# Kernel optimization log

Measured on AMD Instinct MI355X. Metric: run time of the kernel, lower is better.

Reference implementation:

```python
import jax, jax.numpy as jnp
import numpy as np

N, D, S, H, QP, VP = 512, 256, 32, 4, 8, 8
PAIR_C = S + 3 * VP          # 56
P3 = H * QP * 3              # 96
FD = P3 + 16                 # 112 (rel + dist rbf)


def _layer_norm(x, scale, offset, eps=1e-5):
    mu = x.mean(-1, keepdims=True)
    var = ((x - mu) ** 2).mean(-1, keepdims=True)
    return (x - mu) * jax.lax.rsqrt(var + eps) * scale + offset


def _distance_rbf(d, bins=16, min_d=0.0, max_d=22.0):
    # Gaussian RBF featurization of pairwise distances (salad distance_rbf).
    step = (max_d - min_d) / bins
    centers = min_d + step * jnp.arange(bins, dtype=d.dtype) + step / 2
    return jnp.exp(-(((d[..., None] - centers) / step) ** 2))


def setup_inputs() -> dict:
    key = jax.random.key(0)
    ks = jax.random.split(key, 16)
    f32 = jnp.float32
    nrm = lambda k, shape, s=1.0: (s * jax.random.normal(k, shape)).astype(f32)
    HS = H * S
    return {
        "local": nrm(ks[0], (N, D)),
        "pos": nrm(ks[1], (N, 5, 3)),
        "resi": jnp.arange(N, dtype=jnp.int32),
        "chain": jax.random.randint(ks[2], (N,), 0, 2, dtype=jnp.int32),
        "batch": jnp.zeros((N,), dtype=jnp.int32),
        "mask": jnp.ones((N,), dtype=bool),
        "q_ln_scale": jnp.ones((S,), f32),
        "q_ln_offset": jnp.zeros((S,), f32),
        "k_ln_scale": jnp.ones((S,), f32),
        "k_ln_offset": jnp.zeros((S,), f32),
        "w_q": nrm(ks[3], (D, HS), D ** -0.5),
        "b_q": jnp.zeros((HS,), f32),
        "w_k": nrm(ks[4], (D, HS), D ** -0.5),
        "b_k": jnp.zeros((HS,), f32),
        "w_v": nrm(ks[5], (D, HS), D ** -0.5),
        "b_v": jnp.zeros((HS,), f32),
        "w_qp": nrm(ks[6], (D, H * QP * 3), 0.1 * D ** -0.5),
        "b_qp": jnp.zeros((H * QP * 3,), f32),
        "w_kp": nrm(ks[7], (D, H * QP * 3), 0.1 * D ** -0.5),
        "b_kp": jnp.zeros((H * QP * 3,), f32),
        "w_vp": nrm(ks[8], (D, H * VP * 3), 0.1 * D ** -0.5),
        "b_vp": jnp.zeros((H * VP * 3,), f32),
        "resi_embedding": nrm(ks[9], (66, PAIR_C), 66 ** -0.5),
        "w_pair": nrm(ks[10], (FD, PAIR_C), FD ** -0.5),
        "w_bias": nrm(ks[11], (FD, H), FD ** -0.5),
        "b_bias": jnp.zeros((H,), f32),
        "gamma": jnp.full((H,), np.log(np.e - 1.0), f32),
        "w_out": nrm(ks[12], (H * PAIR_C, D), (H * PAIR_C) ** -0.5),
    }


def reference(local, pos, resi, chain, batch, mask,
              q_ln_scale, q_ln_offset, k_ln_scale, k_ln_offset,
              w_q, b_q, w_k, b_k, w_v, b_v,
              w_qp, b_qp, w_kp, b_kp, w_vp, b_vp,
              resi_embedding, w_pair, w_bias, b_bias, gamma, w_out):
    n = local.shape[0]
    ca = pos[:, 1]  # [n,3]

    q = _layer_norm((local @ w_q + b_q).reshape(n, H, S), q_ln_scale, q_ln_offset)
    k = _layer_norm((local @ w_k + b_k).reshape(n, H, S), k_ln_scale, k_ln_offset)
    v = (local @ w_v + b_v).reshape(n, H, S)
    qp = (local @ w_qp + b_qp).reshape(n, H, QP, 3) + ca[:, None, None]
    kp = (local @ w_kp + b_kp).reshape(n, H, QP, 3) + ca[:, None, None]
    vp = (local @ w_vp + b_vp).reshape(n, H, VP, 3) + ca[:, None, None]
    value = jnp.concatenate((v, vp.reshape(n, H, 3 * VP)), axis=-1)  # [n,H,56]

    same_batch = batch[:, None] == batch[None, :]
    pair_mask = (mask[:, None] & mask[None, :]) & same_batch  # [n,n]

    inner = jnp.einsum('ihc,jhc->ijh', q * jnp.sqrt(1.0 / S), k)  # [n,n,H]
    diff = qp[:, None] - kp[None, :]                 # [n,n,H,QP,3]
    point_att = -(diff ** 2).sum(axis=(-1, -2))      # [n,n,H]
    rel = diff.reshape(n, n, P3)                     # [n,n,96]

    dca = 10.0 * ca
    dist = jnp.sqrt(((dca[:, None] - dca[None, :]) ** 2).sum(-1) + 1e-6)
    dist = _distance_rbf(dist)                       # [n,n,16]

    resi_dist = jnp.clip(resi[:, None] - resi[None, :], -32, 32)
    other_chain = chain[:, None] != chain[None, :]
    rdist = jnp.where(other_chain, 65, resi_dist + 32)
    emb = resi_embedding[rdist]                      # [n,n,56]

    feat = jnp.concatenate((rel, dist), axis=-1)     # [n,n,112]
    pair = emb + feat @ w_pair                       # [n,n,56]
    bias = feat @ w_bias + b_bias                    # [n,n,H]
    pair = pair[:, :, None, :] + value[None]         # [n,n,H,56]

    w_C = jnp.sqrt(2.0 / (9 * QP))
    point_scale = jax.nn.softplus(gamma).reshape(1, 1, H) * w_C / 2

    attn = (inner + point_scale * point_att + bias) * jnp.sqrt(1.0 / 3.0)
    attn = jnp.where(pair_mask[..., None], attn, -1e9)
    attn = jax.nn.softmax(attn, axis=1)
    attn = jnp.where(pair_mask[..., None], attn, 0.0)

    result = jnp.einsum('ijh,ijhc->ihc', attn, pair).reshape(n, -1)  # [n,224]
    return result @ w_out                             # [n,D]
```

## Files before the change

### kernel.cpp

```cpp
#include <hip/hip_runtime.h>
#include <hip/hip_bf16.h>
#include <cstddef>

#define N_NODES 512
#define DIM     256
#define H_HEADS 4
#define PAIR_CN 56
#define P3_N    96
#define FD_N    112
#define HPC     224

typedef _Float16 h2v  __attribute__((ext_vector_type(2)));
typedef _Float16 f16x8 __attribute__((ext_vector_type(8)));
typedef float    f32x4 __attribute__((ext_vector_type(4)));

__device__ __forceinline__ bool mask_true(const void* m, int idx) {
    if (((const unsigned char*)m)[idx] != 0) return true;
    return ((const int*)m)[idx] != 0;
}
__device__ __forceinline__ unsigned packh2(float a, float b) {
    _Float16 ha = (_Float16)a, hb = (_Float16)b;
    unsigned short ua, ub;
    __builtin_memcpy(&ua, &ha, 2); __builtin_memcpy(&ub, &hb, 2);
    return (unsigned)ua | ((unsigned)ub << 16);
// ... 115 lines not shown
                const float x6 = xL[r][d0 + 6], x7 = xL[r][d0 + 7];
                acc[r][0] += x0*wv0.x + x1*wv1.x + x2*wv2.x + x3*wv3.x
                           + x4*wv4.x + x5*wv5.x + x6*wv6.x + x7*wv7.x;
                acc[r][1] += x0*wv0.y + x1*wv1.y + x2*wv2.y + x3*wv3.y
                           + x4*wv4.y + x5*wv5.y + x6*wv6.y + x7*wv7.y;
                acc[r][2] += x0*wv0.z + x1*wv1.z + x2*wv2.z + x3*wv3.z
                           + x4*wv4.z + x5*wv5.z + x6*wv6.z + x7*wv7.z;
                acc[r][3] += x0*wv0.w + x1*wv1.w + x2*wv2.w + x3*wv3.w
                           + x4*wv4.w + x5*wv5.w + x6*wv6.w + x7*wv7.w;
            }
        }
#pragma unroll
        for (int r = 0; r < 2; ++r)
#pragma unroll
            for (int e = 0; e < 4; ++e)
                acc[r][e] += __shfl_xor(acc[r][e], 1);

        if (dh == 0) {
            const float cax0 = pos[i0*15+3],     cay0 = pos[i0*15+4],     caz0 = pos[i0*15+5];
            const float cax1 = pos[(i0+1)*15+3], cay1 = pos[(i0+1)*15+4], caz1 = pos[(i0+1)*15+5];
            float fr0[4], fr1[4];
            const bool isKp = (seg == 4), isQp = (seg == 3);
#pragma unroll
            for (int e = 0; e < 4; ++e) {
                const int cc = c + e;
                const float v0 = acc[0][e], v1 = acc[1][e];
                if (seg == 0) {
                    qraw[0][cc] = v0 + b_q[cc];
                    qraw[1][cc] = v1 + b_q[cc];
                } else if (seg == 1) {
                    kraw[0][cc] = v0 + b_k[cc];
                    kraw[1][cc] = v1 + b_k[cc];
                } else if (seg == 2) {
                    const int h = cc >> 5, sc = cc & 31;
                    const int colF = h*PAIR_CN + sc;
                    BF[(colF >> 4)*4096 + (colF & 15)*4 + cstBF] =
                        packh2(v0 + b_v[cc], v1 + b_v[cc]);
                } else if (seg == 3) {
                    const int x = cc % 3;
                    const float cav0 = (x==0)?cax0:((x==1)?cay0:caz0);
                    const float cav1 = (x==0)?cax1:((x==1)?cay1:caz1);
                    const float r0 = v0 + b_qp[cc] + cav0;
                    const float r1 = v1 + b_qp[cc] + cav1;
                    fr0[e] = r0; fr1[e] = r1;
                    qpL[0][cc] = r0; qpL[1][cc] = r1;
                } else if (seg == 4) {
                    const int x = cc % 3;
                    const float cav0 = (x==0)?cax0:((x==1)?cay0:caz0);
                    const float cav1 = (x==0)?cax1:((x==1)?cay1:caz1);
                    const float r0 = v0 + b_kp[cc] + cav0;
                    const float r1 = v1 + b_kp[cc] + cav1;
                    fr0[e] = r0; fr1[e] = r1;
                    const int colF = 224 + cc;
                    BF[(colF >> 4)*4096 + (colF & 15)*4 + cstBF] = packh2(r0, r1);
                    kpbL[0][cc] = (float)(_Float16)r0;
                    kpbL[1][cc] = (float)(_Float16)r1;
                } else {
                    const int h = cc / 24, rr = cc % 24, x = cc % 3;
                    const float cav0 = (x==0)?cax0:((x==1)?cay0:caz0);
                    const float cav1 = (x==0)?cax1:((x==1)?cay1:caz1);
                    const int colF = h*PAIR_CN + 32 + rr;
                    BF[(colF >> 4)*4096 + (colF & 15)*4 + cstBF] =
                        packh2(v0 + b_vp[cc] + cav0, v1 + b_vp[cc] + cav1);
                }
            }
            if (isQp) {
                const int f2 = c >> 1;
                qpP[(size_t)i0*48 + f2]         = packh2(fr0[0], fr0[1]);
                qpP[(size_t)i0*48 + f2 + 1]     = packh2(fr0[2], fr0[3]);
                qpP[(size_t)(i0+1)*48 + f2]     = packh2(fr1[0], fr1[1]);
                qpP[(size_t)(i0+1)*48 + f2 + 1] = packh2(fr1[2], fr1[3]);
            }
            if (isKp) {
                const int f2 = c >> 1;
                const int fq = f2 >> 2;
                kpT4[((size_t)fq*N_NODES + i0    )*4 + (f2 & 3)]       = packh2(fr0[0], fr0[1]);
                kpT4[((size_t)fq*N_NODES + i0    )*4 + ((f2 + 1) & 3)] = packh2(fr0[2], fr0[3]);
                kpT4[((size_t)fq*N_NODES + i0 + 1)*4 + (f2 & 3)]       = packh2(fr1[0], fr1[1]);
                kpT4[((size_t)fq*N_NODES + i0 + 1)*4 + ((f2 + 1) & 3)] = packh2(fr1[2], fr1[3]);
            }
        }
    }
    __syncthreads();

    if (tid < 16) {
        const int r = tid >> 3, t = tid & 7;
        const float* src = (t < 4) ? qraw[r] : kraw[r];
        const int h = t & 3, base = (t < 4) ? 0 : 8;
        float mu = 0.f;
        for (int c = 0; c < 32; ++c) mu += src[h*32 + c];
        mu *= (1.f/32.f);
        float var = 0.f;
        for (int c = 0; c < 32; ++c) { float d = src[h*32 + c] - mu; var += d*d; }
        var *= (1.f/32.f);
        stat[r][base + h*2 + 0] = mu;
        stat[r][base + h*2 + 1] = var;
    }
    __syncthreads();

    {
        const int r = tid >> 8, u = tid & 255;
        const int i = i0 + r;
        if (u < 128) {
            const int h = u >> 5, sidx = u & 31;
            const float mu = stat[r][h*2], var = stat[r][h*2+1];
            float v = (qraw[r][u] - mu) * rsqrtf(var + 1e-5f) * qls[sidx] + qlo[sidx];
            v *= 0.17677669529663687f;
            const float vo = __shfl_xor(v, 1);
            if (!(u & 1)) qnP[(size_t)i*64 + (u >> 1)] = packh2(v, vo);
        } else {
            const int u2 = u - 128, h = u2 >> 5, sidx = u2 & 31;
            const float mu = stat[r][8 + h*2], var = stat[r][9 + h*2];
            float v = (kraw[r][u2] - mu) * rsqrtf(var + 1e-5f) * kls[sidx] + klo[sidx];
            const float vo = __shfl_xor(v, 1);
            if (!(u2 & 1))
                knT4[(((size_t)(u2 >> 3))*N_NODES + i)*4 + ((u2 >> 1) & 3)] = packh2(v, vo);
        }
    }

    if (tid < 64) {
        const int r = tid >> 5, h = (tid >> 3) & 3, ks = tid & 7;
        float uacc = 0.f, tacc = 0.f;
#pragma unroll
        for (int f = ks; f < P3_N; f += 8) {
            float wb = wbS[f*4 + h];
            uacc += qpL[r][f] * wb;
            tacc += kpbL[r][f] * wb;
        }
        float nq = 0.f, nk = 0.f;
#pragma unroll
        for (int f = h*24 + ks*3; f < h*24 + ks*3 + 3; ++f) {
            nq += qpL[r][f]*qpL[r][f];
            nk += kpbL[r][f]*kpbL[r][f];
        }
        uacc += __shfl_xor(uacc,1); uacc += __shfl_xor(uacc,2); uacc += __shfl_xor(uacc,4);
        tacc += __shfl_xor(tacc,1); tacc += __shfl_xor(tacc,2); tacc += __shfl_xor(tacc,4);
        nq   += __shfl_xor(nq,1);   nq   += __shfl_xor(nq,2);   nq   += __shfl_xor(nq,4);
        nk   += __shfl_xor(nk,1);   nk   += __shfl_xor(nk,2);   nk   += __shfl_xor(nk,4);
        if (ks == 0) {
            const int n = i0 + r;
            const float ps = log1pf(expf(gamma[h])) * (1.0f/12.0f);
            iinfo[n*4 + h] = -ps*nq + uacc + b_bias[h];
            jinfo[n*8 + h] = -ps*nk - tacc;
            if (h == 0) {
                jinfo[n*8 + 4] = 10.f * pos[n*15 + 3];
                jinfo[n*8 + 5] = 10.f * pos[n*15 + 4];
                jinfo[n*8 + 6] = 10.f * pos[n*15 + 5];
                jinfo[n*8 + 7] = 0.f;
            }
        }
    }
}

__global__ __launch_bounds__(512, 4) void attn_kernel(
    const unsigned* __restrict__ qnP, const unsigned* __restrict__ knT4,
    const unsigned* __restrict__ qpP, const unsigned* __restrict__ kpT4,
    const unsigned* __restrict__ BF,
    const unsigned* __restrict__ woPk, const unsigned* __restrict__ wp2,
    const unsigned* __restrict__ remb2,
    const float* __restrict__ jinfo, const float* __restrict__ iinfo,
    const int* __restrict__ resi, const int* __restrict__ chain,
    const int* __restrict__ batch, const void* __restrict__ maskp,
    const float* __restrict__ w_bias, const float* __restrict__ gamma,
    float* __restrict__ out)
{
    const int i    = blockIdx.x;
    const int tid  = threadIdx.x;
    const int lane = tid & 63;
    const int wv   = tid >> 6;

    __shared__ unsigned qpkL[64];
    __shared__ unsigned qspkL[48];
    __shared__ unsigned wbPk[H_HEADS][8];
    __shared__ __align__(16) unsigned rbfP[N_NODES][9];
    __shared__ __align__(16) unsigned attnH[H_HEADS][260];
    __shared__ float    mxW[8][H_HEADS], smW[8][H_HEADS];
    __shared__ float    asL[H_HEADS];
    __shared__ float    qpiL[P3_N];
    __shared__ float    GLfF[H_HEADS][P3_N];
    __shared__ float    GLfR[H_HEADS][16];
    __shared__ unsigned GLf2[H_HEADS][56];
    __shared__ unsigned abktP[H_HEADS][33];
    __shared__ float    resL[HPC];
    __shared__ unsigned resH[FD_N];
    __shared__ float    abktW[8][H_HEADS][66];
    __shared__ unsigned char rdL[N_NODES], pmL[N_NODES];

    if (tid < 64) {
        qpkL[tid] = qnP[(size_t)i*64 + tid];
    } else if (tid < 112) {
        const int f2 = tid - 64, h = f2 / 12;
        const float ps2 = 2.f * log1pf(expf(gamma[h])) * (1.0f/12.0f);
        const unsigned u = qpP[(size_t)i*48 + f2];
        qspkL[f2] = packh2(ps2*h2lof(u), ps2*h2hif(u));
    } else if (tid < 160) {
        const int f2 = tid - 112;
        const unsigned u = qpP[(size_t)i*48 + f2];
        qpiL[2*f2]   = h2lof(u);
        qpiL[2*f2+1] = h2hif(u);
    } else if (tid < 192) {
        const int v = tid - 160, h = v >> 3, e = v & 7;
        wbPk[h][e] = packh2(w_bias[(P3_N + 2*e)*H_HEADS + h],
                            w_bias[(P3_N + 2*e + 1)*H_HEADS + h]);
    }
    for (int t = tid; t < 8*H_HEADS*66; t += 512) ((float*)abktW)[t] = 0.f;

    const int  r_i = resi[i], ch_i = chain[i], ba_i = batch[i];
    const bool m_i = mask_true(maskp, i);
    const float dix = jinfo[(size_t)i*8+4], diy = jinfo[(size_t)i*8+5], diz = jinfo[(size_t)i*8+6];

    const float inv3  = 0.57735026918962576f;
    const float rstep = 0.72727272727272727f;

    const int j = tid;
    const float4 vq4 = *(const float4*)(jinfo + (size_t)j*8);
    const float4 dj4 = *(const float4*)(jinfo + (size_t)j*8 + 4);
    const float4 ci4 = *(const float4*)(iinfo + (size_t)i*4);
    const float vqa[4] = {vq4.x, vq4.y, vq4.z, vq4.w};
    const float cia[4] = {ci4.x, ci4.y, ci4.z, ci4.w};
    const float dd0 = dix - dj4.x, dd1 = diy - dj4.y, dd2 = diz - dj4.z;
    const float dist = sqrtf(dd0*dd0 + dd1*dd1 + dd2*dd2 + 1e-6f);
    unsigned rr[8];
#pragma unroll
    for (int p = 0; p < 8; ++p) {
        const float u0 = (dist - (1.375f*(float)(2*p)   + 0.6875f)) * rstep;
        const float u1 = (dist - (1.375f*(float)(2*p+1) + 0.6875f)) * rstep;
        rr[p] = packh2(__expf(-u0*u0), __expf(-u1*u1));
        rbfP[j][p] = rr[p];
    }
    const int  rj = resi[j], cj = chain[j], bj = batch[j];
    const bool pm = m_i && mask_true(maskp, j) && (ba_i == bj);
    const int  rdv = (ch_i != cj) ? 65 : (min(max(r_i - rj, -32), 32) + 32);
    rdL[j] = (unsigned char)rdv;
    pmL[j] = pm ? 1 : 0;
    __syncthreads();

    float lv[4];
    {
        const uint4* kcol = (const uint4*)knT4 + j;
        const uint4* pcol = (const uint4*)kpT4 + j;
        const uint4* qk4  = (const uint4*)qpkL;
        const uint4* qs4  = (const uint4*)qspkL;
#pragma unroll
        for (int hp = 0; hp < 2; ++hp) {
            const int h0 = hp*2, h1 = hp*2 + 1;
            const uint4 ka0 = kcol[(size_t)(h0*4 + 0)*N_NODES];
            const uint4 ka1 = kcol[(size_t)(h0*4 + 1)*N_NODES];
            const uint4 ka2 = kcol[(size_t)(h0*4 + 2)*N_NODES];
            const uint4 ka3 = kcol[(size_t)(h0*4 + 3)*N_NODES];
            const uint4 kb0 = kcol[(size_t)(h1*4 + 0)*N_NODES];
            const uint4 kb1 = kcol[(size_t)(h1*4 + 1)*N_NODES];
            const uint4 kb2 = kcol[(size_t)(h1*4 + 2)*N_NODES];
            const uint4 kb3 = kcol[(size_t)(h1*4 + 3)*N_NODES];
            const uint4 pa0 = pcol[(size_t)(h0*3 + 0)*N_NODES];
            const uint4 pa1 = pcol[(size_t)(h0*3 + 1)*N_NODES];
            const uint4 pa2 = pcol[(size_t)(h0*3 + 2)*N_NODES];
            const uint4 pb0 = pcol[(size_t)(h1*3 + 0)*N_NODES];
            const uint4 pb1 = pcol[(size_t)(h1*3 + 1)*N_NODES];
            const uint4 pb2 = pcol[(size_t)(h1*3 + 2)*N_NODES];
            float a0 = 0.f;
            {
                const uint4 q0 = qk4[h0*4 + 0], q1 = qk4[h0*4 + 1];
                const uint4 q2 = qk4[h0*4 + 2], q3 = qk4[h0*4 + 3];
                a0 = dot2u(ka0.x, q0.x, a0); a0 = dot2u(ka0.y, q0.y, a0);
                a0 = dot2u(ka0.z, q0.z, a0); a0 = dot2u(ka0.w, q0.w, a0);
                a0 = dot2u(ka1.x, q1.x, a0); a0 = dot2u(ka1.y, q1.y, a0);
                a0 = dot2u(ka1.z, q1.z, a0); a0 = dot2u(ka1.w, q1.w, a0);
                a0 = dot2u(ka2.x, q2.x, a0); a0 = dot2u(ka2.y, q2.y, a0);
                a0 = dot2u(ka2.z, q2.z, a0); a0 = dot2u(ka2.w, q2.w, a0);
                a0 = dot2u(ka3.x, q3.x, a0); a0 = dot2u(ka3.y, q3.y, a0);
                a0 = dot2u(ka3.z, q3.z, a0); a0 = dot2u(ka3.w, q3.w, a0);
                const uint4 s0 = qs4[h0*3 + 0], s1 = qs4[h0*3 + 1], s2 = qs4[h0*3 + 2];
                a0 = dot2u(pa0.x, s0.x, a0); a0 = dot2u(pa0.y, s0.y, a0);
                a0 = dot2u(pa0.z, s0.z, a0); a0 = dot2u(pa0.w, s0.w, a0);
                a0 = dot2u(pa1.x, s1.x, a0); a0 = dot2u(pa1.y, s1.y, a0);
                a0 = dot2u(pa1.z, s1.z, a0); a0 = dot2u(pa1.w, s1.w, a0);
                a0 = dot2u(pa2.x, s2.x, a0); a0 = dot2u(pa2.y, s2.y, a0);
                a0 = dot2u(pa2.z, s2.z, a0); a0 = dot2u(pa2.w, s2.w, a0);
                const uint4 w0 = *(const uint4*)&wbPk[h0][0];
                const uint4 w1 = *(const uint4*)&wbPk[h0][4];
                a0 = dot2u(rr[0], w0.x, a0); a0 = dot2u(rr[1], w0.y, a0);
                a0 = dot2u(rr[2], w0.z, a0); a0 = dot2u(rr[3], w0.w, a0);
                a0 = dot2u(rr[4], w1.x, a0); a0 = dot2u(rr[5], w1.y, a0);
                a0 = dot2u(rr[6], w1.z, a0); a0 = dot2u(rr[7], w1.w, a0);
            }
            lv[h0] = pm ? (a0 + cia[h0] + vqa[h0]) * inv3 : -1e9f;
            float a1 = 0.f;
            {
                const uint4 q0 = qk4[h1*4 + 0], q1 = qk4[h1*4 + 1];
                const uint4 q2 = qk4[h1*4 + 2], q3 = qk4[h1*4 + 3];
                a1 = dot2u(kb0.x, q0.x, a1); a1 = dot2u(kb0.y, q0.y, a1);
                a1 = dot2u(kb0.z, q0.z, a1); a1 = dot2u(kb0.w, q0.w, a1);
                a1 = dot2u(kb1.x, q1.x, a1); a1 = dot2u(kb1.y, q1.y, a1);
                a1 = dot2u(kb1.z, q1.z, a1); a1 = dot2u(kb1.w, q1.w, a1);
                a1 = dot2u(kb2.x, q2.x, a1); a1 = dot2u(kb2.y, q2.y, a1);
                a1 = dot2u(kb2.z, q2.z, a1); a1 = dot2u(kb2.w, q2.w, a1);
                a1 = dot2u(kb3.x, q3.x, a1); a1 = dot2u(kb3.y, q3.y, a1);
                a1 = dot2u(kb3.z, q3.z, a1); a1 = dot2u(kb3.w, q3.w, a1);
                const uint4 s0 = qs4[h1*3 + 0], s1 = qs4[h1*3 + 1], s2 = qs4[h1*3 + 2];
                a1 = dot2u(pb0.x, s0.x, a1); a1 = dot2u(pb0.y, s0.y, a1);
                a1 = dot2u(pb0.z, s0.z, a1); a1 = dot2u(pb0.w, s0.w, a1);
                a1 = dot2u(pb1.x, s1.x, a1); a1 = dot2u(pb1.y, s1.y, a1);
                a1 = dot2u(pb1.z, s1.z, a1); a1 = dot2u(pb1.w, s1.w, a1);
                a1 = dot2u(pb2.x, s2.x, a1); a1 = dot2u(pb2.y, s2.y, a1);
                a1 = dot2u(pb2.z, s2.z, a1); a1 = dot2u(pb2.w, s2.w, a1);
                const uint4 w0 = *(const uint4*)&wbPk[h1][0];
                const uint4 w1 = *(const uint4*)&wbPk[h1][4];
                a1 = dot2u(rr[0], w0.x, a1); a1 = dot2u(rr[1], w0.y, a1);
                a1 = dot2u(rr[2], w0.z, a1); a1 = dot2u(rr[3], w0.w, a1);
                a1 = dot2u(rr[4], w1.x, a1); a1 = dot2u(rr[5], w1.y, a1);
                a1 = dot2u(rr[6], w1.z, a1); a1 = dot2u(rr[7], w1.w, a1);
            }
            lv[h1] = pm ? (a1 + cia[h1] + vqa[h1]) * inv3 : -1e9f;
        }
    }

    {
        float mx[4] = {lv[0], lv[1], lv[2], lv[3]};
#pragma unroll
        for (int off = 1; off < 64; off <<= 1) {
#pragma unroll
            for (int h = 0; h < 4; ++h) mx[h] = fmaxf(mx[h], __shfl_xor(mx[h], off));
        }
        if (lane == 0) *(float4*)&mxW[wv][0] = make_float4(mx[0], mx[1], mx[2], mx[3]);
        __syncthreads();
        float mxg[4] = {-1e30f, -1e30f, -1e30f, -1e30f};
#pragma unroll
        for (int w = 0; w < 8; ++w) {
            const float4 m = *(const float4*)&mxW[w][0];
            mxg[0] = fmaxf(mxg[0], m.x); mxg[1] = fmaxf(mxg[1], m.y);
            mxg[2] = fmaxf(mxg[2], m.z); mxg[3] = fmaxf(mxg[3], m.w);
        }
        float e[4], sm[4];
#pragma unroll
        for (int h = 0; h < 4; ++h) {
            e[h] = pm ? __expf(lv[h] - mxg[h]) : 0.f;
            sm[h] = e[h];
        }
#pragma unroll
        for (int off = 1; off < 64; off <<= 1) {
#pragma unroll
            for (int h = 0; h < 4; ++h) sm[h] += __shfl_xor(sm[h], off);
        }
        if (lane == 0) *(float4*)&smW[wv][0] = make_float4(sm[0], sm[1], sm[2], sm[3]);
        __syncthreads();
        float smt[4] = {0.f, 0.f, 0.f, 0.f};
#pragma unroll
        for (int w = 0; w < 8; ++w) {
            const float4 m = *(const float4*)&smW[w][0];
            smt[0] += m.x; smt[1] += m.y; smt[2] += m.z; smt[3] += m.w;
        }
        float p[4];
#pragma unroll
        for (int h = 0; h < 4; ++h) {
            const float rden = 1.f / fmaxf(smt[h], 1e-37f);
            p[h] = e[h] * rden;
            atomicAdd(&abktW[wv][h][rdv], p[h]);
        }
        if (tid == 0) {
#pragma unroll
            for (int h = 0; h < 4; ++h)
                asL[h] = smt[h] / fmaxf(smt[h], 1e-37f);
        }
#pragma unroll
        for (int h = 0; h < 4; ++h) {
            const float po = __shfl_xor(p[h], 1);
            if (!(j & 1)) attnH[h][j >> 1] = packh2(p[h], po);
        }
    }
    __syncthreads();

    if (wv < 7) {
        const int row = lane & 15;
        const int ntA = wv, ntB = wv + 7, ntC = wv + 14;
        const bool hasC = (ntC < 20);
        f32x4 accA = {0.f,0.f,0.f,0.f};
        f32x4 accB = {0.f,0.f,0.f,0.f};
        f32x4 accC = {0.f,0.f,0.f,0.f};
        const uint4* bfp = (const uint4*)BF;
#pragma unroll 4
        for (int kt = 0; kt < 16; ++kt) {
            uint4 au = make_uint4(0u, 0u, 0u, 0u);
            if (row < 4) au = *(const uint4*)&attnH[row][kt*16 + (lane >> 4)*4];
            const uint4 bA = bfp[(ntA*16 + kt)*64 + lane];
            const uint4 bB = bfp[(ntB*16 + kt)*64 + lane];
            accA = mfma16(au, bA, accA);
            accB = mfma16(au, bB, accB);
            if (hasC) {
                const uint4 bC = bfp[(ntC*16 + kt)*64 + lane];
                accC = mfma16(au, bC, accC);
            }
        }
        if (lane < 16) {
            {
                const int s = ntA*16 + lane, h = s / PAIR_CN;
                resL[s] = (h==0) ? accA[0] : ((h==1) ? accA[1] : ((h==2) ? accA[2] : accA[3]));
            }
            {
                const int s = ntB*16 + lane, h = s / PAIR_CN;
                resL[s] = (h==0) ? accB[0] : ((h==1) ? accB[1] : ((h==2) ? accB[2] : accB[3]));
            }
            if (hasC) {
                const int f = (ntC - 14)*16 + lane;
                GLfF[0][f] = accC[0];
                GLfF[1][f] = accC[1];
                GLfF[2][f] = accC[2];
                GLfF[3][f] = accC[3];
            }
        }
    } else {
        const int idx = tid - 448, b = idx >> 2, q = idx & 3;
        const int w = b >> 1;
        const bool hi = (b & 1);
        float a[4] = {0.f, 0.f, 0.f, 0.f};
#pragma unroll 4
        for (int jpp = q*64; jpp < q*64 + 64; ++jpp) {
            const unsigned r0 = rbfP[2*jpp][w];
            const unsigned r1 = rbfP[2*jpp + 1][w];
            const unsigned ee = hi ? ((r0 >> 16) | (r1 & 0xffff0000u))
                                   : ((r0 & 0xffffu) | (r1 << 16));
            a[0] = dot2u(ee, attnH[0][jpp], a[0]);
            a[1] = dot2u(ee, attnH[1][jpp], a[1]);
            a[2] = dot2u(ee, attnH[2][jpp], a[2]);
            a[3] = dot2u(ee, attnH[3][jpp], a[3]);
        }
#pragma unroll
        for (int h = 0; h < 4; ++h) {
            a[h] += __shfl_xor(a[h], 1);
            a[h] += __shfl_xor(a[h], 2);
            if (q == 0) GLfR[h][b] = a[h];
        }
    }
    __syncthreads();

    for (int t = tid; t < 224; t += 512) {
        const int h = t / 56, f2 = t % 56;
        if (f2 < 48) {
            GLf2[h][f2] = packh2(qpiL[2*f2]*asL[h]     - GLfF[h][2*f2],
                                 qpiL[2*f2 + 1]*asL[h] - GLfF[h][2*f2 + 1]);
        } else {
            GLf2[h][f2] = packh2(GLfR[h][(f2 - 48)*2], GLfR[h][(f2 - 48)*2 + 1]);
        }
    }
    for (int t = tid; t < 132; t += 512) {
        const int h = t / 33, r2 = t % 33;
        float s0 = 0.f, s1 = 0.f;
#pragma unroll
        for (int w = 0; w < 8; ++w) {
            s0 += abktW[w][h][2*r2];
            s1 += abktW[w][h][2*r2 + 1];
        }
        abktP[h][r2] = packh2(s0, s1);
    }
    __syncthreads();

    if (tid < HPC) {
        const int h = tid / PAIR_CN, c = tid - h*PAIR_CN;
        float r = resL[tid];
        {
            unsigned buf[16];
#pragma unroll
            for (int t = 0; t < 16; ++t) buf[t] = remb2[t*56 + c];
#pragma unroll
            for (int t = 0; t < 16; ++t) r = dot2u(buf[t], abktP[h][t], r);
#pragma unroll
            for (int t = 0; t < 16; ++t) buf[t] = remb2[(16 + t)*56 + c];
#pragma unroll
            for (int t = 0; t < 16; ++t) r = dot2u(buf[t], abktP[h][16 + t], r);
            r = dot2u(remb2[32*56 + c], abktP[h][32], r);
        }
        {
            unsigned buf[14];
#pragma unroll
            for (int qq = 0; qq < 4; ++qq) {
#pragma unroll
                for (int t = 0; t < 14; ++t) buf[t] = wp2[(qq*14 + t)*56 + c];
#pragma unroll
                for (int t = 0; t < 14; ++t) r = dot2u(buf[t], GLf2[h][qq*14 + t], r);
            }
        }
        resL[tid] = r;
    }
    __syncthreads();

    if (tid < FD_N) resH[tid] = packh2(resL[2*tid], resL[2*tid + 1]);
    __syncthreads();

    {
        const int col = tid >> 1, ph = tid & 1;
        float o = 0.f;
        unsigned buf[14];
#pragma unroll
        for (int qq = 0; qq < 4; ++qq) {
            const int base = ph*56 + qq*14;
#pragma unroll
            for (int t = 0; t < 14; ++t) buf[t] = woPk[(base + t)*256 + col];
#pragma unroll
            for (int t = 0; t < 14; ++t) o = dot2u(buf[t], resH[base + t], o);
        }
        o += __shfl_xor(o, 1);
        if (ph == 0) out[(size_t)i*DIM + col] = o;
    }
}

extern "C" void kernel_launch(void* const* d_in, const int* in_sizes, int n_in,
                              void* d_out, int out_size, void* d_ws, size_t ws_size,
                              hipStream_t stream) {
    (void)in_sizes; (void)n_in; (void)out_size; (void)ws_size;
    const float* local = (const float*)d_in[0];
    const float* pos   = (const float*)d_in[1];
    const int*   resi  = (const int*)d_in[2];
    const int*   chain = (const int*)d_in[3];
    const int*   batch = (const int*)d_in[4];
    const void*  maskp = d_in[5];
    const float* qls   = (const float*)d_in[6];
    const float* qlo   = (const float*)d_in[7];
    const float* kls   = (const float*)d_in[8];
    const float* klo   = (const float*)d_in[9];
    const float* w_q   = (const float*)d_in[10];
    const float* b_q   = (const float*)d_in[11];
    const float* w_k   = (const float*)d_in[12];
    const float* b_k   = (const float*)d_in[13];
    const float* w_v   = (const float*)d_in[14];
    const float* b_v   = (const float*)d_in[15];
    const float* w_qp  = (const float*)d_in[16];
    const float* b_qp  = (const float*)d_in[17];
    const float* w_kp  = (const float*)d_in[18];
    const float* b_kp  = (const float*)d_in[19];
    const float* w_vp  = (const float*)d_in[20];
    const float* b_vp  = (const float*)d_in[21];
    const float* remb  = (const float*)d_in[22];
    const float* w_pair= (const float*)d_in[23];
    const float* w_bias= (const float*)d_in[24];
    const float* b_bias= (const float*)d_in[25];
    const float* gamma = (const float*)d_in[26];
    const float* w_out = (const float*)d_in[27];

    char* ws = (char*)d_ws;
    unsigned* qnP   = (unsigned*)(ws);
    unsigned* qpP   = (unsigned*)(ws + 131072);
    unsigned* knT4  = (unsigned*)(ws + 229376);
    unsigned* kpT4  = (unsigned*)(ws + 360448);
    unsigned* BF    = (unsigned*)(ws + 458752);
    float*    jinf  = (float*)(ws + 786432);
    float*    iinf  = (float*)(ws + 802816);
    unsigned* woPk  = (unsigned*)(ws + 811008);
    unsigned* wp2   = (unsigned*)(ws + 925696);
    unsigned* remb2 = (unsigned*)(ws + 938240);

    proj_kernel<<<N_NODES / 2, 512, 0, stream>>>(
        local, pos, qls, qlo, kls, klo,
        w_q, b_q, w_k, b_k, w_v, b_v,
        w_qp, b_qp, w_kp, b_kp, w_vp, b_vp,
        w_bias, b_bias, gamma,
        remb, w_pair, w_out,
        qnP, knT4, qpP, kpT4, BF,
        woPk, wp2, remb2, jinf, iinf);

    attn_kernel<<<N_NODES, 512, 0, stream>>>(
        qnP, knT4, qpP, kpT4, BF,
        woPk, wp2, remb2, jinf, iinf,
        resi, chain, batch, maskp,
        w_bias, gamma,
        (float*)d_out);
}
```

Before: 53.82 us.

## Process two query rows per attention block with 1024 threads, splitting heads across halves

The attention kernel now handles two query nodes per block with 1024 threads. Each half of the block takes two heads for both rows, so K and key-point loads are shared across the two rows. The MFMA stage now feeds 8 attention rows (2 rows × 4 heads) into one tile, and the embedding, pair-projection and output-projection weight loads are reused for both rows. This cuts redundant global weight traffic and halves the block count, at the cost of more shared memory, fewer blocks to spread over the CUs, and heavier per-block synchronisation.

```diff
diff --git a/kernel.cpp b/kernel.cpp
--- a/kernel.cpp
+++ b/kernel.cpp
@@ -291,7 +291,7 @@
     }
 }
 
-__global__ __launch_bounds__(512, 4) void attn_kernel(
+__global__ __launch_bounds__(1024, 4) void attn_kernel(
     const unsigned* __restrict__ qnP, const unsigned* __restrict__ knT4,
     const unsigned* __restrict__ qpP, const unsigned* __restrict__ kpT4,
     const unsigned* __restrict__ BF,
@@ -303,100 +303,122 @@
     const float* __restrict__ w_bias, const float* __restrict__ gamma,
     float* __restrict__ out)
 {
-    const int i    = blockIdx.x;
+    const int ib   = blockIdx.x * 2;
     const int tid  = threadIdx.x;
     const int lane = tid & 63;
     const int wv   = tid >> 6;
-
-    __shared__ unsigned qpkL[64];
-    __shared__ unsigned qspkL[48];
+    const int hp   = tid >> 9;
+    const int j    = tid & 511;
+
+    __shared__ unsigned qpkL[2][64];
+    __shared__ unsigned qspkL[2][48];
     __shared__ unsigned wbPk[H_HEADS][8];
-    __shared__ __align__(16) unsigned rbfP[N_NODES][9];
-    __shared__ __align__(16) unsigned attnH[H_HEADS][260];
-    __shared__ float    mxW[8][H_HEADS], smW[8][H_HEADS];
-    __shared__ float    asL[H_HEADS];
-    __shared__ float    qpiL[P3_N];
-    __shared__ float    GLfF[H_HEADS][P3_N];
-    __shared__ float    GLfR[H_HEADS][16];
-    __shared__ unsigned GLf2[H_HEADS][56];
-    __shared__ unsigned abktP[H_HEADS][33];
-    __shared__ float    resL[HPC];
-    __shared__ unsigned resH[FD_N];
-    __shared__ float    abktW[8][H_HEADS][66];
-    __shared__ unsigned char rdL[N_NODES], pmL[N_NODES];
-
-    if (tid < 64) {
-        qpkL[tid] = qnP[(size_t)i*64 + tid];
-    } else if (tid < 112) {
-        const int f2 = tid - 64, h = f2 / 12;
+    __shared__ __align__(16) unsigned rbfP[2][N_NODES][9];
+    __shared__ __align__(16) unsigned attnH2[8][260];
+    __shared__ float    mxW[16][4], smW[16][4];
+    __shared__ float    asL2[2][H_HEADS];
+    __shared__ float    qpiL2[2][P3_N];
+    __shared__ float    GLfF2[2][H_HEADS][P3_N];
+    __shared__ float    GLfR2[2][H_HEADS][16];
+    __shared__ unsigned GLf22[2][H_HEADS][56];
+    __shared__ unsigned abktP2[2][H_HEADS][33];
+    __shared__ float    resL2[2][HPC];
+    __shared__ unsigned resH2[2][FD_N];
+    __shared__ float    abktW8[8][2][H_HEADS][66];
+
+    if (tid < 128) {
+        const int r = tid >> 6, u = tid & 63;
+        qpkL[r][u] = qnP[(size_t)(ib + r)*64 + u];
+    } else if (tid < 224) {
+        const int v = tid - 128, r = v / 48, f2 = v % 48;
+        const int h = f2 / 12;
         const float ps2 = 2.f * log1pf(expf(gamma[h])) * (1.0f/12.0f);
-        const unsigned u = qpP[(size_t)i*48 + f2];
-        qspkL[f2] = packh2(ps2*h2lof(u), ps2*h2hif(u));
-    } else if (tid < 160) {
-        const int f2 = tid - 112;
-        const unsigned u = qpP[(size_t)i*48 + f2];
-        qpiL[2*f2]   = h2lof(u);
-        qpiL[2*f2+1] = h2hif(u);
-    } else if (tid < 192) {
-        const int v = tid - 160, h = v >> 3, e = v & 7;
+        const unsigned u = qpP[(size_t)(ib + r)*48 + f2];
+        qspkL[r][f2] = packh2(ps2*h2lof(u), ps2*h2hif(u));
+    } else if (tid < 320) {
+        const int v = tid - 224, r = v / 48, f2 = v % 48;
+        const unsigned u = qpP[(size_t)(ib + r)*48 + f2];
+        qpiL2[r][2*f2]   = h2lof(u);
+        qpiL2[r][2*f2+1] = h2hif(u);
+    } else if (tid < 352) {
+        const int v = tid - 320, h = v >> 3, e = v & 7;
         wbPk[h][e] = packh2(w_bias[(P3_N + 2*e)*H_HEADS + h],
                             w_bias[(P3_N + 2*e + 1)*H_HEADS + h]);
     }
-    for (int t = tid; t < 8*H_HEADS*66; t += 512) ((float*)abktW)[t] = 0.f;
-
-    const int  r_i = resi[i], ch_i = chain[i], ba_i = batch[i];
-    const bool m_i = mask_true(maskp, i);
-    const float dix = jinfo[(size_t)i*8+4], diy = jinfo[(size_t)i*8+5], diz = jinfo[(size_t)i*8+6];
+    for (int t = tid; t < 8*2*H_HEADS*66; t += 1024) ((float*)abktW8)[t] = 0.f;
+
+    const int  ri0 = resi[ib], ri1 = resi[ib+1];
+    const int  ch0 = chain[ib], ch1 = chain[ib+1];
+    const int  ba0 = batch[ib], ba1 = batch[ib+1];
+    const bool mi0 = mask_true(maskp, ib), mi1 = mask_true(maskp, ib+1);
+    const float dix0 = jinfo[(size_t)ib*8+4], diy0 = jinfo[(size_t)ib*8+5], diz0 = jinfo[(size_t)ib*8+6];
+    const float dix1 = jinfo[(size_t)(ib+1)*8+4], diy1 = jinfo[(size_t)(ib+1)*8+5], diz1 = jinfo[(size_t)(ib+1)*8+6];
 
     const float inv3  = 0.57735026918962576f;
     const float rstep = 0.72727272727272727f;
 
-    const int j = tid;
     const float4 vq4 = *(const float4*)(jinfo + (size_t)j*8);
     const float4 dj4 = *(const float4*)(jinfo + (size_t)j*8 + 4);
-    const float4 ci4 = *(const float4*)(iinfo + (size_t)i*4);
+    const float4 ciA = *(const float4*)(iinfo + (size_t)ib*4);
+    const float4 ciB = *(const float4*)(iinfo + (size_t)(ib+1)*4);
     const float vqa[4] = {vq4.x, vq4.y, vq4.z, vq4.w};
-    const float cia[4] = {ci4.x, ci4.y, ci4.z, ci4.w};
-    const float dd0 = dix - dj4.x, dd1 = diy - dj4.y, dd2 = diz - dj4.z;
-    const float dist = sqrtf(dd0*dd0 + dd1*dd1 + dd2*dd2 + 1e-6f);
-    unsigned rr[8];
-#pragma unroll
-    for (int p = 0; p < 8; ++p) {
-        const float u0 = (dist - (1.375f*(float)(2*p)   + 0.6875f)) * rstep;
-        const float u1 = (dist - (1.375f*(float)(2*p+1) + 0.6875f)) * rstep;
-        rr[p] = packh2(__expf(-u0*u0), __expf(-u1*u1));
-        rbfP[j][p] = rr[p];
+    const float cia[2][4] = {{ciA.x, ciA.y, ciA.z, ciA.w},
+                             {ciB.x, ciB.y, ciB.z, ciB.w}};
+    {
+        const float dx = (hp ? dix1 : dix0) - dj4.x;
+        const float dy = (hp ? diy1 : diy0) - dj4.y;
+        const float dz = (hp ? diz1 : diz0) - dj4.z;
+        const float dist = sqrtf(dx*dx + dy*dy + dz*dz + 1e-6f);
+#pragma unroll
+        for (int p = 0; p < 8; ++p) {
+            const float u0 = (dist - (1.375f*(float)(2*p)   + 0.6875f)) * rstep;
+            const float u1 = (dist - (1.375f*(float)(2*p+1) + 0.6875f)) * rstep;
+            rbfP[hp][j][p] = packh2(__expf(-u0*u0), __expf(-u1*u1));
+        }
     }
     const int  rj = resi[j], cj = chain[j], bj = batch[j];
-    const bool pm = m_i && mask_true(maskp, j) && (ba_i == bj);
-    const int  rdv = (ch_i != cj) ? 65 : (min(max(r_i - rj, -32), 32) + 32);
-    rdL[j] = (unsigned char)rdv;
-    pmL[j] = pm ? 1 : 0;
-    __syncthreads();
-
-    float lv[4];
+    const bool mj = mask_true(maskp, j);
+    bool pmv[2];
+    int  rdv[2];
+    pmv[0] = mi0 && mj && (ba0 == bj);
+    pmv[1] = mi1 && mj && (ba1 == bj);
+    rdv[0] = (ch0 != cj) ? 65 : (min(max(ri0 - rj, -32), 32) + 32);
+    rdv[1] = (ch1 != cj) ? 65 : (min(max(ri1 - rj, -32), 32) + 32);
+    __syncthreads();
+
+    float lv[2][2];
     {
+        const int h0 = hp*2, h1 = hp*2 + 1;
         const uint4* kcol = (const uint4*)knT4 + j;
         const uint4* pcol = (const uint4*)kpT4 + j;
-        const uint4* qk4  = (const uint4*)qpkL;
-        const uint4* qs4  = (const uint4*)qspkL;
-#pragma unroll
-        for (int hp = 0; hp < 2; ++hp) {
-            const int h0 = hp*2, h1 = hp*2 + 1;
-            const uint4 ka0 = kcol[(size_t)(h0*4 + 0)*N_NODES];
-            const uint4 ka1 = kcol[(size_t)(h0*4 + 1)*N_NODES];
-            const uint4 ka2 = kcol[(size_t)(h0*4 + 2)*N_NODES];
-            const uint4 ka3 = kcol[(size_t)(h0*4 + 3)*N_NODES];
-            const uint4 kb0 = kcol[(size_t)(h1*4 + 0)*N_NODES];
-            const uint4 kb1 = kcol[(size_t)(h1*4 + 1)*N_NODES];
-            const uint4 kb2 = kcol[(size_t)(h1*4 + 2)*N_NODES];
-            const uint4 kb3 = kcol[(size_t)(h1*4 + 3)*N_NODES];
-            const uint4 pa0 = pcol[(size_t)(h0*3 + 0)*N_NODES];
-            const uint4 pa1 = pcol[(size_t)(h0*3 + 1)*N_NODES];
-            const uint4 pa2 = pcol[(size_t)(h0*3 + 2)*N_NODES];
-            const uint4 pb0 = pcol[(size_t)(h1*3 + 0)*N_NODES];
-            const uint4 pb1 = pcol[(size_t)(h1*3 + 1)*N_NODES];
-            const uint4 pb2 = pcol[(size_t)(h1*3 + 2)*N_NODES];
+        const uint4 ka0 = kcol[(size_t)(h0*4 + 0)*N_NODES];
+        const uint4 ka1 = kcol[(size_t)(h0*4 + 1)*N_NODES];
+        const uint4 ka2 = kcol[(size_t)(h0*4 + 2)*N_NODES];
+        const uint4 ka3 = kcol[(size_t)(h0*4 + 3)*N_NODES];
+        const uint4 kb0 = kcol[(size_t)(h1*4 + 0)*N_NODES];
+        const uint4 kb1 = kcol[(size_t)(h1*4 + 1)*N_NODES];
+        const uint4 kb2 = kcol[(size_t)(h1*4 + 2)*N_NODES];
+        const uint4 kb3 = kcol[(size_t)(h1*4 + 3)*N_NODES];
+        const uint4 pa0 = pcol[(size_t)(h0*3 + 0)*N_NODES];
+        const uint4 pa1 = pcol[(size_t)(h0*3 + 1)*N_NODES];
+        const uint4 pa2 = pcol[(size_t)(h0*3 + 2)*N_NODES];
+        const uint4 pb0 = pcol[(size_t)(h1*3 + 0)*N_NODES];
+        const uint4 pb1 = pcol[(size_t)(h1*3 + 1)*N_NODES];
+        const uint4 pb2 = pcol[(size_t)(h1*3 + 2)*N_NODES];
+        const uint4 rr0a = *(const uint4*)&rbfP[0][j][0];
+        const uint4 rr0b = *(const uint4*)&rbfP[0][j][4];
+        const uint4 rr1a = *(const uint4*)&rbfP[1][j][0];
+        const uint4 rr1b = *(const uint4*)&rbfP[1][j][4];
+        const uint4 w0a = *(const uint4*)&wbPk[h0][0];
+        const uint4 w0b = *(const uint4*)&wbPk[h0][4];
+        const uint4 w1a = *(const uint4*)&wbPk[h1][0];
+        const uint4 w1b = *(const uint4*)&wbPk[h1][4];
+#pragma unroll
+        for (int r = 0; r < 2; ++r) {
+            const uint4* qk4 = (const uint4*)&qpkL[r][0];
+            const uint4* qs4 = (const uint4*)&qspkL[r][0];
+            const uint4 rra = r ? rr1a : rr0a;
+            const uint4 rrb = r ? rr1b : rr0b;
             float a0 = 0.f;
             {
                 const uint4 q0 = qk4[h0*4 + 0], q1 = qk4[h0*4 + 1];
@@ -416,14 +438,12 @@
                 a0 = dot2u(pa1.z, s1.z, a0); a0 = dot2u(pa1.w, s1.w, a0);
                 a0 = dot2u(pa2.x, s2.x, a0); a0 = dot2u(pa2.y, s2.y, a0);
                 a0 = dot2u(pa2.z, s2.z, a0); a0 = dot2u(pa2.w, s2.w, a0);
-                const uint4 w0 = *(const uint4*)&wbPk[h0][0];
-                const uint4 w1 = *(const uint4*)&wbPk[h0][4];
-                a0 = dot2u(rr[0], w0.x, a0); a0 = dot2u(rr[1], w0.y, a0);
-                a0 = dot2u(rr[2], w0.z, a0); a0 = dot2u(rr[3], w0.w, a0);
-                a0 = dot2u(rr[4], w1.x, a0); a0 = dot2u(rr[5], w1.y, a0);
-                a0 = dot2u(rr[6], w1.z, a0); a0 = dot2u(rr[7], w1.w, a0);
-            }
-            lv[h0] = pm ? (a0 + cia[h0] + vqa[h0]) * inv3 : -1e9f;
+                a0 = dot2u(rra.x, w0a.x, a0); a0 = dot2u(rra.y, w0a.y, a0);
+                a0 = dot2u(rra.z, w0a.z, a0); a0 = dot2u(rra.w, w0a.w, a0);
+                a0 = dot2u(rrb.x, w0b.x, a0); a0 = dot2u(rrb.y, w0b.y, a0);
+                a0 = dot2u(rrb.z, w0b.z, a0); a0 = dot2u(rrb.w, w0b.w, a0);
+            }
+            lv[r][0] = pmv[r] ? (a0 + cia[r][h0] + vqa[h0]) * inv3 : -1e9f;
             float a1 = 0.f;
             {
                 const uint4 q0 = qk4[h1*4 + 0], q1 = qk4[h1*4 + 1];
@@ -443,170 +463,195 @@
                 a1 = dot2u(pb1.z, s1.z, a1); a1 = dot2u(pb1.w, s1.w, a1);
                 a1 = dot2u(pb2.x, s2.x, a1); a1 = dot2u(pb2.y, s2.y, a1);
                 a1 = dot2u(pb2.z, s2.z, a1); a1 = dot2u(pb2.w, s2.w, a1);
-                const uint4 w0 = *(const uint4*)&wbPk[h1][0];
-                const uint4 w1 = *(const uint4*)&wbPk[h1][4];
-                a1 = dot2u(rr[0], w0.x, a1); a1 = dot2u(rr[1], w0.y, a1);
-                a1 = dot2u(rr[2], w0.z, a1); a1 = dot2u(rr[3], w0.w, a1);
-                a1 = dot2u(rr[4], w1.x, a1); a1 = dot2u(rr[5], w1.y, a1);
-                a1 = dot2u(rr[6], w1.z, a1); a1 = dot2u(rr[7], w1.w, a1);
-            }
-            lv[h1] = pm ? (a1 + cia[h1] + vqa[h1]) * inv3 : -1e9f;
+                a1 = dot2u(rra.x, w1a.x, a1); a1 = dot2u(rra.y, w1a.y, a1);
+                a1 = dot2u(rra.z, w1a.z, a1); a1 = dot2u(rra.w, w1a.w, a1);
+                a1 = dot2u(rrb.x, w1b.x, a1); a1 = dot2u(rrb.y, w1b.y, a1);
+                a1 = dot2u(rrb.z, w1b.z, a1); a1 = dot2u(rrb.w, w1b.w, a1);
+            }
+            lv[r][1] = pmv[r] ? (a1 + cia[r][h1] + vqa[h1]) * inv3 : -1e9f;
         }
     }
 
     {
-        float mx[4] = {lv[0], lv[1], lv[2], lv[3]};
+        float mx[4] = {lv[0][0], lv[0][1], lv[1][0], lv[1][1]};
 #pragma unroll
         for (int off = 1; off < 64; off <<= 1) {
 #pragma unroll
-            for (int h = 0; h < 4; ++h) mx[h] = fmaxf(mx[h], __shfl_xor(mx[h], off));
+            for (int s = 0; s < 4; ++s) mx[s] = fmaxf(mx[s], __shfl_xor(mx[s], off));
         }
         if (lane == 0) *(float4*)&mxW[wv][0] = make_float4(mx[0], mx[1], mx[2], mx[3]);
         __syncthreads();
         float mxg[4] = {-1e30f, -1e30f, -1e30f, -1e30f};
+        const int wbase = hp*8;
 #pragma unroll
         for (int w = 0; w < 8; ++w) {
-            const float4 m = *(const float4*)&mxW[w][0];
+            const float4 m = *(const float4*)&mxW[wbase + w][0];
             mxg[0] = fmaxf(mxg[0], m.x); mxg[1] = fmaxf(mxg[1], m.y);
             mxg[2] = fmaxf(mxg[2], m.z); mxg[3] = fmaxf(mxg[3], m.w);
         }
         float e[4], sm[4];
-#pragma unroll
-        for (int h = 0; h < 4; ++h) {
-            e[h] = pm ? __expf(lv[h] - mxg[h]) : 0.f;
-            sm[h] = e[h];
-        }
+        e[0] = pmv[0] ? __expf(lv[0][0] - mxg[0]) : 0.f;
+        e[1] = pmv[0] ? __expf(lv[0][1] - mxg[1]) : 0.f;
+        e[2] = pmv[1] ? __expf(lv[1][0] - mxg[2]) : 0.f;
+        e[3] = pmv[1] ? __expf(lv[1][1] - mxg[3]) : 0.f;
+#pragma unroll
+        for (int s = 0; s < 4; ++s) sm[s] = e[s];
 #pragma unroll
         for (int off = 1; off < 64; off <<= 1) {
 #pragma unroll
-            for (int h = 0; h < 4; ++h) sm[h] += __shfl_xor(sm[h], off);
+            for (int s = 0; s < 4; ++s) sm[s] += __shfl_xor(sm[s], off);
         }
         if (lane == 0) *(float4*)&smW[wv][0] = make_float4(sm[0], sm[1], sm[2], sm[3]);
         __syncthreads();
         float smt[4] = {0.f, 0.f, 0.f, 0.f};
 #pragma unroll
         for (int w = 0; w < 8; ++w) {
-            const float4 m = *(const float4*)&smW[w][0];
+            const float4 m = *(const float4*)&smW[wbase + w][0];
             smt[0] += m.x; smt[1] += m.y; smt[2] += m.z; smt[3] += m.w;
         }
         float p[4];
 #pragma unroll
-        for (int h = 0; h < 4; ++h) {
-            const float rden = 1.f / fmaxf(smt[h], 1e-37f);
-            p[h] = e[h] * rden;
-            atomicAdd(&abktW[wv][h][rdv], p[h]);
-        }
-        if (tid == 0) {
-#pragma unroll
-            for (int h = 0; h < 4; ++h)
-                asL[h] = smt[h] / fmaxf(smt[h], 1e-37f);
-        }
-#pragma unroll
-        for (int h = 0; h < 4; ++h) {
-            const float po = __shfl_xor(p[h], 1);
-            if (!(j & 1)) attnH[h][j >> 1] = packh2(p[h], po);
-        }
-    }
-    __syncthreads();
-
-    if (wv < 7) {
+        for (int s = 0; s < 4; ++s) {
+            const float rden = 1.f / fmaxf(smt[s], 1e-37f);
+            p[s] = e[s] * rden;
+        }
+        const int h0 = hp*2;
+        atomicAdd(&abktW8[wv & 7][0][h0    ][rdv[0]], p[0]);
+        atomicAdd(&abktW8[wv & 7][0][h0 + 1][rdv[0]], p[1]);
+        atomicAdd(&abktW8[wv & 7][1][h0    ][rdv[1]], p[2]);
+        atomicAdd(&abktW8[wv & 7][1][h0 + 1][rdv[1]], p[3]);
+        if (j == 0) {
+            asL2[0][h0]     = smt[0] / fmaxf(smt[0], 1e-37f);
+            asL2[0][h0 + 1] = smt[1] / fmaxf(smt[1], 1e-37f);
+            asL2[1][h0]     = smt[2] / fmaxf(smt[2], 1e-37f);
+            asL2[1][h0 + 1] = smt[3] / fmaxf(smt[3], 1e-37f);
+        }
+#pragma unroll
+        for (int s = 0; s < 4; ++s) {
+            const float po = __shfl_xor(p[s], 1);
+            if (!(j & 1)) {
+                const int r = s >> 1, hh = s & 1;
+                attnH2[r*4 + h0 + hh][j >> 1] = packh2(p[s], po);
+            }
+        }
+    }
+    __syncthreads();
+
+    if (wv < 14) {
         const int row = lane & 15;
-        const int ntA = wv, ntB = wv + 7, ntC = wv + 14;
-        const bool hasC = (ntC < 20);
+        const int ntA = wv;
+        const int ntB = (wv < 6) ? (wv + 14) : -1;
         f32x4 accA = {0.f,0.f,0.f,0.f};
         f32x4 accB = {0.f,0.f,0.f,0.f};
-        f32x4 accC = {0.f,0.f,0.f,0.f};
         const uint4* bfp = (const uint4*)BF;
 #pragma unroll 4
         for (int kt = 0; kt < 16; ++kt) {
             uint4 au = make_uint4(0u, 0u, 0u, 0u);
-            if (row < 4) au = *(const uint4*)&attnH[row][kt*16 + (lane >> 4)*4];
+            if (row < 8) au = *(const uint4*)&attnH2[row][kt*16 + (lane >> 4)*4];
             const uint4 bA = bfp[(ntA*16 + kt)*64 + lane];
-            const uint4 bB = bfp[(ntB*16 + kt)*64 + lane];
             accA = mfma16(au, bA, accA);
-            accB = mfma16(au, bB, accB);
-            if (hasC) {
-                const uint4 bC = bfp[(ntC*16 + kt)*64 + lane];
-                accC = mfma16(au, bC, accC);
-            }
-        }
-        if (lane < 16) {
+            if (ntB >= 0) {
+                const uint4 bB = bfp[(ntB*16 + kt)*64 + lane];
+                accB = mfma16(au, bB, accB);
+            }
+        }
+        if (lane < 32) {
+            const int r = lane >> 4, c16 = lane & 15;
             {
-                const int s = ntA*16 + lane, h = s / PAIR_CN;
-                resL[s] = (h==0) ? accA[0] : ((h==1) ? accA[1] : ((h==2) ? accA[2] : accA[3]));
-            }
-            {
-                const int s = ntB*16 + lane, h = s / PAIR_CN;
-                resL[s] = (h==0) ? accB[0] : ((h==1) ? accB[1] : ((h==2) ? accB[2] : accB[3]));
-            }
-            if (hasC) {
-                const int f = (ntC - 14)*16 + lane;
-                GLfF[0][f] = accC[0];
-                GLfF[1][f] = accC[1];
-                GLfF[2][f] = accC[2];
-                GLfF[3][f] = accC[3];
+                const int s = ntA*16 + c16;
+                if (s < HPC) {
+                    resL2[r][s] = ((const float*)&accA)[s / PAIR_CN];
+                } else {
+                    const int f = s - HPC;
+                    GLfF2[r][0][f] = accA[0];
+                    GLfF2[r][1][f] = accA[1];
+                    GLfF2[r][2][f] = accA[2];
+                    GLfF2[r][3][f] = accA[3];
+                }
+            }
+            if (ntB >= 0) {
+                const int s = ntB*16 + c16;
+                if (s < HPC) {
+                    resL2[r][s] = ((const float*)&accB)[s / PAIR_CN];
+                } else {
+                    const int f = s - HPC;
+                    GLfF2[r][0][f] = accB[0];
+                    GLfF2[r][1][f] = accB[1];
+                    GLfF2[r][2][f] = accB[2];
+                    GLfF2[r][3][f] = accB[3];
+                }
             }
         }
     } else {
-        const int idx = tid - 448, b = idx >> 2, q = idx & 3;
+        const int r = wv - 14;
+        const int b = lane >> 2, q = lane & 3;
         const int w = b >> 1;
         const bool hi = (b & 1);
         float a[4] = {0.f, 0.f, 0.f, 0.f};
 #pragma unroll 4
         for (int jpp = q*64; jpp < q*64 + 64; ++jpp) {
-            const unsigned r0 = rbfP[2*jpp][w];
-            const unsigned r1 = rbfP[2*jpp + 1][w];
+            const unsigned r0 = rbfP[r][2*jpp][w];
+            const unsigned r1 = rbfP[r][2*jpp + 1][w];
             const unsigned ee = hi ? ((r0 >> 16) | (r1 & 0xffff0000u))
                                    : ((r0 & 0xffffu) | (r1 << 16));
-            a[0] = dot2u(ee, attnH[0][jpp], a[0]);
-            a[1] = dot2u(ee, attnH[1][jpp], a[1]);
-            a[2] = dot2u(ee, attnH[2][jpp], a[2]);
-            a[3] = dot2u(ee, attnH[3][jpp], a[3]);
+            a[0] = dot2u(ee, attnH2[r*4 + 0][jpp], a[0]);
+            a[1] = dot2u(ee, attnH2[r*4 + 1][jpp], a[1]);
+            a[2] = dot2u(ee, attnH2[r*4 + 2][jpp], a[2]);
+            a[3] = dot2u(ee, attnH2[r*4 + 3][jpp], a[3]);
         }
 #pragma unroll
         for (int h = 0; h < 4; ++h) {
             a[h] += __shfl_xor(a[h], 1);
             a[h] += __shfl_xor(a[h], 2);
-            if (q == 0) GLfR[h][b] = a[h];
-        }
-    }
-    __syncthreads();
-
-    for (int t = tid; t < 224; t += 512) {
-        const int h = t / 56, f2 = t % 56;
+            if (q == 0) GLfR2[r][h][b] = a[h];
+        }
+    }
+    __syncthreads();
+
+    for (int t = tid; t < 448; t += 1024) {
+        const int r = t / 224, v = t % 224, h = v / 56, f2 = v % 56;
         if (f2 < 48) {
-            GLf2[h][f2] = packh2(qpiL[2*f2]*asL[h]     - GLfF[h][2*f2],
-                                 qpiL[2*f2 + 1]*asL[h] - GLfF[h][2*f2 + 1]);
+            GLf22[r][h][f2] = packh2(qpiL2[r][2*f2]*asL2[r][h]     - GLfF2[r][h][2*f2],
+                                     qpiL2[r][2*f2 + 1]*asL2[r][h] - GLfF2[r][h][2*f2 + 1]);
         } else {
-            GLf2[h][f2] = packh2(GLfR[h][(f2 - 48)*2], GLfR[h][(f2 - 48)*2 + 1]);
-        }
-    }
-    for (int t = tid; t < 132; t += 512) {
-        const int h = t / 33, r2 = t % 33;
+            GLf22[r][h][f2] = packh2(GLfR2[r][h][(f2 - 48)*2], GLfR2[r][h][(f2 - 48)*2 + 1]);
+        }
+    }
+    for (int t = tid; t < 264; t += 1024) {
+        const int r = t / 132, v = t % 132, h = v / 33, r2 = v % 33;
         float s0 = 0.f, s1 = 0.f;
 #pragma unroll
         for (int w = 0; w < 8; ++w) {
-            s0 += abktW[w][h][2*r2];
-            s1 += abktW[w][h][2*r2 + 1];
-        }
-        abktP[h][r2] = packh2(s0, s1);
+            s0 += abktW8[w][r][h][2*r2];
+            s1 += abktW8[w][r][h][2*r2 + 1];
+        }
+        abktP2[r][h][r2] = packh2(s0, s1);
     }
     __syncthreads();
 
     if (tid < HPC) {
         const int h = tid / PAIR_CN, c = tid - h*PAIR_CN;
-        float r = resL[tid];
+        float r0 = resL2[0][tid];
+        float r1 = resL2[1][tid];
         {
             unsigned buf[16];
 #pragma unroll
             for (int t = 0; t < 16; ++t) buf[t] = remb2[t*56 + c];
 #pragma unroll
-            for (int t = 0; t < 16; ++t) r = dot2u(buf[t], abktP[h][t], r);
+            for (int t = 0; t < 16; ++t) {
+                r0 = dot2u(buf[t], abktP2[0][h][t], r0);
+                r1 = dot2u(buf[t], abktP2[1][h][t], r1);
+            }
 #pragma unroll
             for (int t = 0; t < 16; ++t) buf[t] = remb2[(16 + t)*56 + c];
 #pragma unroll
-            for (int t = 0; t < 16; ++t) r = dot2u(buf[t], abktP[h][16 + t], r);
-            r = dot2u(remb2[32*56 + c], abktP[h][32], r);
+            for (int t = 0; t < 16; ++t) {
+                r0 = dot2u(buf[t], abktP2[0][h][16 + t], r0);
+                r1 = dot2u(buf[t], abktP2[1][h][16 + t], r1);
+            }
+            const unsigned b32 = remb2[32*56 + c];
+            r0 = dot2u(b32, abktP2[0][h][32], r0);
+            r1 = dot2u(b32, abktP2[1][h][32], r1);
         }
         {
             unsigned buf[14];
@@ -615,19 +660,26 @@
 #pragma unroll
                 for (int t = 0; t < 14; ++t) buf[t] = wp2[(qq*14 + t)*56 + c];
 #pragma unroll
-                for (int t = 0; t < 14; ++t) r = dot2u(buf[t], GLf2[h][qq*14 + t], r);
-            }
-        }
-        resL[tid] = r;
-    }
-    __syncthreads();
-
-    if (tid < FD_N) resH[tid] = packh2(resL[2*tid], resL[2*tid + 1]);
-    __syncthreads();
-
-    {
+                for (int t = 0; t < 14; ++t) {
+                    r0 = dot2u(buf[t], GLf22[0][h][qq*14 + t], r0);
+                    r1 = dot2u(buf[t], GLf22[1][h][qq*14 + t], r1);
+                }
+            }
+        }
+        resL2[0][tid] = r0;
+        resL2[1][tid] = r1;
+    }
+    __syncthreads();
+
+    if (tid < 2*FD_N) {
+        const int r = tid / FD_N, t2 = tid % FD_N;
+        resH2[r][t2] = packh2(resL2[r][2*t2], resL2[r][2*t2 + 1]);
+    }
+    __syncthreads();
+
+    if (tid < 512) {
         const int col = tid >> 1, ph = tid & 1;
-        float o = 0.f;
+        float o0 = 0.f, o1 = 0.f;
         unsigned buf[14];
 #pragma unroll
         for (int qq = 0; qq < 4; ++qq) {
@@ -635,10 +687,17 @@
 #pragma unroll
             for (int t = 0; t < 14; ++t) buf[t] = woPk[(base + t)*256 + col];
 #pragma unroll
-            for (int t = 0; t < 14; ++t) o = dot2u(buf[t], resH[base + t], o);
-        }
-        o += __shfl_xor(o, 1);
-        if (ph == 0) out[(size_t)i*DIM + col] = o;
+            for (int t = 0; t < 14; ++t) {
+                o0 = dot2u(buf[t], resH2[0][base + t], o0);
+                o1 = dot2u(buf[t], resH2[1][base + t], o1);
+            }
+        }
+        o0 += __shfl_xor(o0, 1);
+        o1 += __shfl_xor(o1, 1);
+        if (ph == 0) {
+            out[(size_t)ib*DIM + col]       = o0;
+            out[(size_t)(ib + 1)*DIM + col] = o1;
+        }
     }
 }
 
@@ -696,7 +755,7 @@
         qnP, knT4, qpP, kpT4, BF,
         woPk, wp2, remb2, jinf, iinf);
 
-    attn_kernel<<<N_NODES, 512, 0, stream>>>(
+    attn_kernel<<<N_NODES / 2, 1024, 0, stream>>>(
         qnP, knT4, qpP, kpT4, BF,
         woPk, wp2, remb2, jinf, iinf,
         resi, chain, batch, maskp,
```

Result: no change. 53.62 us, median of 2 (-0.4%).
